# Optimization experiments

Measured on AMD Instinct MI355X. Metric: run time of the kernel, lower is better.

## Reference

```python
import jax, jax.numpy as jnp
import numpy as np
import math

B, S, HID = 2, 2048, 1024
NH = 16
HD = HID // NH  # 64
CHUNK = 128  # min(128, S) from the module


def setup_inputs() -> dict:
    key = jax.random.key(0)
    ks = jax.random.split(key, 8)
    scale = 1.0 / math.sqrt(HID)
    return {
        "hidden_states": jax.random.normal(ks[0], (B, S, HID), jnp.float32),
        "attention_mask": jnp.zeros((B, S, S), jnp.float32),
        "Wq": jax.random.normal(ks[1], (HID, HID), jnp.float32) * scale,
        "bq": jnp.zeros((HID,), jnp.float32),
        "Wk": jax.random.normal(ks[2], (HID, HID), jnp.float32) * scale,
        "bk": jnp.zeros((HID,), jnp.float32),
        "Wv": jax.random.normal(ks[3], (HID, HID), jnp.float32) * scale,
        "bv": jnp.zeros((HID,), jnp.float32),
        "head_weights": jnp.ones((NH,), jnp.float32),
    }


def _split_heads(x):
    # [B,S,HID] -> [B,NH,S,HD]
    b, s, _ = x.shape
    return x.reshape(b, s, NH, HD).transpose(0, 2, 1, 3)


def reference(hidden_states, attention_mask, Wq, bq, Wk, bk, Wv, bv, head_weights):
    # nn.Linear: y = x @ W.T + b
    q = _split_heads(hidden_states @ Wq.T + bq)  # [B,NH,S,HD]
    k = _split_heads(hidden_states @ Wk.T + bk)
    v = _split_heads(hidden_states @ Wv.T + bv)

    scores = jnp.einsum("bhqd,bhkd->bhqk", q, k) / math.sqrt(HD)
    scores = scores + attention_mask[:, None, :, :]  # additive mask broadcast over heads
    probs = jax.nn.softmax(scores, axis=-1)
    # dropout p=0.0 -> identity; post-softmax head-weight scaling (head_pruning)
    probs = probs * head_weights[None, :, None, None]
    ctx = jnp.einsum("bhqk,bhkd->bhqd", probs, v)  # [B,NH,S,HD]
    context_layer = ctx.transpose(0, 2, 1, 3).reshape(B, S, HID)

    # module returns the probs of the LAST query chunk of the python loop
    last_start = ((S + CHUNK - 1) // CHUNK - 1) * CHUNK
    output_attention_probs = probs[:, :, last_start:S, :]  # [B,NH,128,S]
    return context_layer, output_attention_probs
```

## Files before the change

### kernel.cpp

```cpp
#include <hip/hip_runtime.h>

typedef unsigned short u16;
typedef __attribute__((ext_vector_type(8))) short bf16x8;
typedef __attribute__((ext_vector_type(4))) float f32x4;

#define B_   2
#define S_   2048
#define HID_ 1024
#define NH_  16
#define HD_  64
#define SCALE_ 0.125f

__device__ __forceinline__ u16 f2bf(float f) {
    union { float f; unsigned int i; } v; v.f = f;
    unsigned int r = v.i + 0x7fffu + ((v.i >> 16) & 1u);
    return (u16)(r >> 16);
}
__device__ __forceinline__ bf16x8 ld8(const u16* p) {
    return *reinterpret_cast<const bf16x8*>(p);
}
__device__ __forceinline__ unsigned cvtpk(float lo, float hi) {
    unsigned r;
    asm("v_cvt_pk_bf16_f32 %0, %1, %2" : "=v"(r) : "v"(lo), "v"(hi));
    return r;
}
__device__ __forceinline__ void gll16(const u16* g, const u16* l) {
    __builtin_amdgcn_global_load_lds(
        (const __attribute__((address_space(1))) unsigned int*)g,
        (__attribute__((address_space(3))) unsigned int*)l, 16, 0, 0);
}

__global__ __launch_bounds__(256) void conv_scan(
    const float* __restrict__ X, const float* __restrict__ W0,
    const float* __restrict__ W1, const float* __restrict__ W2,
    const unsigned* __restrict__ m,
    u16* __restrict__ Xb, u16* __restrict__ Wb, unsigned* __restrict__ flag)
{
    const int bx = blockIdx.x;
    if (bx < 3584) {
        const size_t s = (size_t)bx * 256 + threadIdx.x;
        const float* src; u16* dst; size_t off;
        if (s < 524288) { src = X; dst = Xb; off = s * 8; }
        else {
            const size_t t = s - 524288;
            const int w = (int)(t >> 17);
            off = (t & 131071) * 8;
            src = w == 0 ? W0 : w == 1 ? W1 : W2;
            dst = Wb + (size_t)w * 1048576;
        }
        f32x4 a = *(const f32x4*)(src + off);
        f32x4 b = *(const f32x4*)(src + off + 4);
        bf16x8 r;
        #pragma unroll
        for (int e = 0; e < 4; e++) { r[e] = (short)f2bf(a[e]); r[4 + e] = (short)f2bf(b[e]); }
        *(bf16x8*)(dst + off) = r;
    } else {
        const size_t i = ((size_t)(bx - 3584) * 256 + threadIdx.x) * 8;
        const uint4* p = (const uint4*)(m + i);
        uint4 a = p[0], b = p[1];
        const unsigned M = 0x7fffffffu;
        unsigned v = (a.x & M) | (a.y & M) | (a.z & M) | (a.w & M)
                   | (b.x & M) | (b.y & M) | (b.z & M) | (b.w & M);
        if (v) atomicOr(flag, 1u);
    }
}

#define BK_ 64

__global__ __launch_bounds__(256) void qkv_mfma(
    const u16* __restrict__ Xb, const u16* __restrict__ Wb,
    const float* __restrict__ bq, const float* __restrict__ bk,
    const float* __restrict__ bv,
    u16* __restrict__ Q, u16* __restrict__ K, u16* __restrict__ V)
{
    __shared__ __align__(16) u16 As[128 * BK_];
    __shared__ __align__(16) u16 Bs[128 * BK_];

    const int tid  = threadIdx.x;
    const int wave = tid >> 6;
    const int lane = tid & 63;
    const int l16  = lane & 15;
    const int quad = lane >> 4;
    const int wr   = wave >> 1, wc = wave & 1;

    const int i0 = blockIdx.x * 128;
    const int j0 = blockIdx.y * 128;

    const int grow = lane >> 3;
    const int gcol = (lane & 7) * 8;

    f32x4 acc[4][4] = {};

    for (int k0 = 0; k0 < HID_; k0 += BK_) {
        __syncthreads();
        #pragma unroll
        for (int g = 0; g < 4; g++) {
            const int u = wave * 4 + g;
            gll16(Xb + (size_t)(i0 + u * 8 + grow) * HID_ + k0 + gcol, As + u * 512);
            gll16(Wb + (size_t)(j0 + u * 8 + grow) * HID_ + k0 + gcol, Bs + u * 512);
        }
        __syncthreads();

        #pragma unroll
        for (int kk = 0; kk < 2; kk++) {
            bf16x8 af[4], bfr[4];
            #pragma unroll
            for (int mt = 0; mt < 4; mt++)
                af[mt] = ld8(&As[(wr * 64 + mt * 16 + l16) * BK_ + kk * 32 + quad * 8]);
            #pragma unroll
            for (int nt = 0; nt < 4; nt++)
                bfr[nt] = ld8(&Bs[(wc * 64 + nt * 16 + l16) * BK_ + kk * 32 + quad * 8]);
            #pragma unroll
            for (int mt = 0; mt < 4; mt++)
                #pragma unroll
                for (int nt = 0; nt < 4; nt++)
                    acc[mt][nt] = __builtin_amdgcn_mfma_f32_16x16x32_bf16(af[mt], bfr[nt], acc[mt][nt], 0, 0, 0);
        }
    }

    const int which = j0 >> 10;
    const float* bias = which == 0 ? bq : which == 1 ? bk : bv;
    u16* Y            = which == 0 ? Q  : which == 1 ? K  : V;

    u16* bb = As + wave * 2048;

    #pragma unroll
    for (int p = 0; p < 2; p++) {
        __syncthreads();
        #pragma unroll
        for (int t2 = 0; t2 < 2; t2++) {
            const int nt = 2 * p + t2;
            const int j  = j0 + wc * 64 + nt * 16 + l16;
            const int jj = j & 1023;
            const float bv_ = bias[jj];
            #pragma unroll
            for (int mt = 0; mt < 4; mt++)
                #pragma unroll
                for (int r = 0; r < 4; r++) {
                    const int row = mt * 16 + quad * 4 + r;
                    const int col = t2 * 16 + l16;
                    const u16 val = f2bf(acc[mt][nt][r] + bv_);
                    if (which == 2)
                        bb[col * 64 + (row ^ ((col & 7) << 3))] = val;
                    else
                        bb[row * 32 + (col ^ ((row & 0xC) << 1))] = val;
                }
        }
        __syncthreads();
        #pragma unroll
        for (int k = 0; k < 4; k++) {
            const int c = lane + 64 * k;
            if (which == 2) {
                const int col  = c >> 3;
                const int row0 = (c & 7) * 8;
                bf16x8 v = ld8(&bb[col * 64 + (row0 ^ ((col & 7) << 3))]);
                const int j  = j0 + wc * 64 + p * 32 + col;
                const int jj = j & 1023;
                const int h = jj >> 6, d = jj & 63;
                const int i = i0 + wr * 64 + row0;
                const int b = i >> 11, s = i & (S_ - 1);
                *(bf16x8*)&Y[((size_t)(b * NH_ + h) * HD_ + d) * S_ + s] = v;
            } else {
                const int row  = c >> 2;
                const int col0 = (c & 3) * 8;
                bf16x8 v = ld8(&bb[row * 32 + (col0 ^ ((row & 0xC) << 1))]);
                const int j  = j0 + wc * 64 + p * 32 + col0;
                const int jj = j & 1023;
                const int h = jj >> 6, d = jj & 63;
                const int i = i0 + wr * 64 + row;
                const int b = i >> 11, s = i & (S_ - 1);
                *(bf16x8*)&Y[(((size_t)(b * NH_ + h) * S_ + s) * HD_) + d] = v;
            }
        }
    }
}

__global__ __launch_bounds__(256) void attn(
    const u16* __restrict__ Q, const u16* __restrict__ K, const u16* __restrict__ Vt,
    const float* __restrict__ mask, const float* __restrict__ hw,
    const unsigned* __restrict__ mflag,
    float* __restrict__ ctx, float* __restrict__ ml)
{
    __shared__ __align__(16) u16 Ks[2][64 * 64];
    __shared__ __align__(16) u16 Vs[2][64 * 64];
    __shared__ __align__(16) u16 Pl[4][16 * 64];

    const int usemask = (mflag[0] != 0);

    const int tid  = threadIdx.x;
    const int wave = tid >> 6;
    const int lane = tid & 63;
    const int l16  = lane & 15;
    const int quad = lane >> 4;
    const int x7   = l16 & 7;

    const int lin = blockIdx.x + 32 * (blockIdx.y + 16 * blockIdx.z);
    const int xcd = lin & 7, jj = lin >> 3;
    const int qb  = jj & 31;
    const int hb  = xcd * 4 + (jj >> 5);
    const int h   = hb & 15, b = hb >> 4;
    const int bh  = b * NH_ + h;

    const u16* Qh  = Q  + (size_t)bh * S_ * HD_;
    const u16* Kh  = K  + (size_t)bh * S_ * HD_;
    const u16* Vth = Vt + (size_t)bh * HD_ * S_;
    const float* Mb = mask + (size_t)b * S_ * S_;

    const int q0 = qb * 64 + wave * 16;

    bf16x8 qf0 = ld8(Qh + (size_t)(q0 + l16) * HD_ + quad * 8);
    bf16x8 qf1 = ld8(Qh + (size_t)(q0 + l16) * HD_ + 32 + quad * 8);

    f32x4 oacc[4] = {};
    float l_part = 0.f;

    const int srow = tid >> 3;
    const int sch  = tid & 7;
    const int ssw  = (sch ^ (srow & 7)) * 8;
    const int sL   = srow * 64 + ssw;

    {
        bf16x8 k0 = ld8(Kh + (size_t)srow * HD_ + sch * 8);
        bf16x8 k1 = ld8(Kh + (size_t)(srow + 32) * HD_ + sch * 8);
        bf16x8 v0 = ld8(Vth + (size_t)srow * S_ + sch * 8);
        bf16x8 v1 = ld8(Vth + (size_t)(srow + 32) * S_ + sch * 8);
        *(bf16x8*)&Ks[0][sL] = k0; *(bf16x8*)&Ks[0][sL + 2048] = k1;
        *(bf16x8*)&Vs[0][sL] = v0; *(bf16x8*)&Vs[0][sL + 2048] = v1;
    }
    __syncthreads();

    for (int t = 0; t < 32; ++t) {
        const int cur = t & 1;
        const int kt  = t * 64;
        const u16* Kb = Ks[cur];
        const u16* Vb = Vs[cur];

        bf16x8 kr0, kr1, vr0, vr1;
        if (t < 31) {
            const u16* Kg = Kh + (size_t)(kt + 64) * HD_;
            kr0 = ld8(Kg + (size_t)srow * HD_ + sch * 8);
            kr1 = ld8(Kg + (size_t)(srow + 32) * HD_ + sch * 8);
            vr0 = ld8(Vth + (size_t)srow * S_ + kt + 64 + sch * 8);
            vr1 = ld8(Vth + (size_t)(srow + 32) * S_ + kt + 64 + sch * 8);
        }

        f32x4 sacc[4] = {};
        __builtin_amdgcn_s_setprio(1);
        #pragma unroll
        for (int nb = 0; nb < 4; nb++) {
            const int base = (nb * 16 + l16) * 64;
            bf16x8 k0 = ld8(&Kb[base + ((quad ^ x7) * 8)]);
            bf16x8 k1 = ld8(&Kb[base + (((quad + 4) ^ x7) * 8)]);
            sacc[nb] = __builtin_amdgcn_mfma_f32_16x16x32_bf16(k0, qf0, sacc[nb], 0, 0, 0);
            sacc[nb] = __builtin_amdgcn_mfma_f32_16x16x32_bf16(k1, qf1, sacc[nb], 0, 0, 0);
        }
        __builtin_amdgcn_s_setprio(0);

        float p[4][4];
        if (usemask) {
            const float* Mrow = Mb + (size_t)(q0 + l16) * S_ + kt;
            #pragma unroll
            for (int nb = 0; nb < 4; nb++) {
                const float4 mv = *(const float4*)(Mrow + nb * 16 + quad * 4);
                p[nb][0] = __expf(fminf(sacc[nb][0] * SCALE_ + mv.x, 80.f));
                p[nb][1] = __expf(fminf(sacc[nb][1] * SCALE_ + mv.y, 80.f));
                p[nb][2] = __expf(fminf(sacc[nb][2] * SCALE_ + mv.z, 80.f));
                p[nb][3] = __expf(fminf(sacc[nb][3] * SCALE_ + mv.w, 80.f));
                l_part += p[nb][0] + p[nb][1] + p[nb][2] + p[nb][3];
            }
        } else {
            #pragma unroll
            for (int nb = 0; nb < 4; nb++) {
                #pragma unroll
                for (int r = 0; r < 4; r++) {
                    p[nb][r] = __expf(fminf(sacc[nb][r] * SCALE_, 80.f));
                    l_part += p[nb][r];
                }
            }
        }

        {
            u16* prow = &Pl[wave][l16 * 64];
            #pragma unroll
            for (int nb = 0; nb < 4; nb++) {
                uint2 w;
                w.x = cvtpk(p[nb][0], p[nb][1]);
                w.y = cvtpk(p[nb][2], p[nb][3]);
                const int ch  = 2 * nb + (quad >> 1);
                const int off = ((ch ^ x7) << 3) + ((quad & 1) << 2);
                *(uint2*)&prow[off] = w;
            }
        }

        __builtin_amdgcn_s_setprio(1);
        #pragma unroll
        for (int kb = 0; kb < 2; kb++) {
            const int c = kb * 4 + quad;
            bf16x8 pf = ld8(&Pl[wave][l16 * 64 + ((c ^ x7) * 8)]);
            #pragma unroll
            for (int db = 0; db < 4; db++) {
                bf16x8 vf = ld8(&Vb[(db * 16 + l16) * 64 + ((c ^ x7) * 8)]);
                oacc[db] = __builtin_amdgcn_mfma_f32_16x16x32_bf16(pf, vf, oacc[db], 0, 0, 0);
            }
        }
        __builtin_amdgcn_s_setprio(0);

        if (t < 31) {
            u16* Kd = Ks[cur ^ 1]; u16* Vd = Vs[cur ^ 1];
            *(bf16x8*)&Kd[sL] = kr0; *(bf16x8*)&Kd[sL + 2048] = kr1;
            *(bf16x8*)&Vd[sL] = vr0; *(bf16x8*)&Vd[sL + 2048] = vr1;
        }
        __syncthreads();
    }

    float lsum = l_part;
    lsum += __shfl_xor(lsum, 16);
    lsum += __shfl_xor(lsum, 32);

    const float hwf  = hw[h];
    const float invq = hwf / lsum;
    float invl[4];
    #pragma unroll
    for (int r = 0; r < 4; r++)
        invl[r] = __shfl(invq, (lane & 48) + quad * 4 + r);

    #pragma unroll
    for (int db = 0; db < 4; db++)
        #pragma unroll
        for (int r = 0; r < 4; r++) {
            const int qrow = q0 + quad * 4 + r;
            ctx[((size_t)(b * S_ + qrow)) * HID_ + h * HD_ + db * 16 + l16] =
                oacc[db][r] * invl[r];
        }

    if (qb >= 30 && quad == 0)
        ml[bh * 128 + (q0 - 1920) + l16] = lsum;
}

__global__ __launch_bounds__(256) void probs_qk(
    const u16* __restrict__ Q, const u16* __restrict__ K,
    const float* __restrict__ mask, const float* __restrict__ hw,
    const unsigned* __restrict__ mflag, const float* __restrict__ ml,
    float* __restrict__ probs_out)
{
    const int usemask = (mflag[0] != 0);

    const int tid  = threadIdx.x;
    const int wave = tid >> 6;
    const int lane = tid & 63;
    const int l16  = lane & 15;
    const int quad = lane >> 4;

    const int rt = blockIdx.x & 1;
    const int ks = blockIdx.x >> 1;
    const int h  = blockIdx.y;
    const int b  = blockIdx.z;
    const int bh = b * NH_ + h;

    const u16* Qh = Q + (size_t)bh * S_ * HD_;
    const u16* Kh = K + (size_t)bh * S_ * HD_;
    const float* Mb = mask + (size_t)b * S_ * S_;

    const int q0   = 1920 + rt * 64 + wave * 16;
    const int qrow = q0 + l16;

    bf16x8 qf0 = ld8(Qh + (size_t)qrow * HD_ + quad * 8);
    bf16x8 qf1 = ld8(Qh + (size_t)qrow * HD_ + 32 + quad * 8);

    const float invl = hw[h] / ml[bh * 128 + (qrow - 1920)];
    float* Prow = probs_out + ((size_t)bh * 128 + (qrow - 1920)) * S_;
    const float* Mrow = Mb + (size_t)qrow * S_;

    for (int kt = ks * 256; kt < ks * 256 + 256; kt += 64) {
        f32x4 sacc[4] = {};
        #pragma unroll
        for (int nb = 0; nb < 4; nb++) {
            const u16* krow = Kh + (size_t)(kt + nb * 16 + l16) * HD_ + quad * 8;
            bf16x8 kA0 = ld8(krow);
            bf16x8 kA1 = ld8(krow + 32);
            sacc[nb] = __builtin_amdgcn_mfma_f32_16x16x32_bf16(kA0, qf0, sacc[nb], 0, 0, 0);
            sacc[nb] = __builtin_amdgcn_mfma_f32_16x16x32_bf16(kA1, qf1, sacc[nb], 0, 0, 0);
        }
        #pragma unroll
        for (int nb = 0; nb < 4; nb++) {
            const int kb0 = kt + nb * 16 + quad * 4;
            float4 v;
            if (usemask) {
                const float4 mv = *(const float4*)&Mrow[kb0];
                v.x = __expf(fminf(sacc[nb][0] * SCALE_ + mv.x, 80.f)) * invl;
                v.y = __expf(fminf(sacc[nb][1] * SCALE_ + mv.y, 80.f)) * invl;
                v.z = __expf(fminf(sacc[nb][2] * SCALE_ + mv.z, 80.f)) * invl;
                v.w = __expf(fminf(sacc[nb][3] * SCALE_ + mv.w, 80.f)) * invl;
            } else {
                v.x = __expf(fminf(sacc[nb][0] * SCALE_, 80.f)) * invl;
                v.y = __expf(fminf(sacc[nb][1] * SCALE_, 80.f)) * invl;
                v.z = __expf(fminf(sacc[nb][2] * SCALE_, 80.f)) * invl;
                v.w = __expf(fminf(sacc[nb][3] * SCALE_, 80.f)) * invl;
            }
            *(float4*)&Prow[kb0] = v;
        }
    }
}

extern "C" void kernel_launch(void* const* d_in, const int* in_sizes, int n_in,
                              void* d_out, int out_size, void* d_ws, size_t ws_size,
                              hipStream_t stream)
{
    const void* X = 0; const void* mask = 0; const void* hw = 0;
    const void* Wm[3] = {0, 0, 0}; const void* bm[3] = {0, 0, 0};
    int wi = 0, bi = 0;
    for (int i = 0; i < n_in; i++) {
        switch (in_sizes[i]) {
            case 4194304: X = d_in[i]; break;
            case 8388608: mask = d_in[i]; break;
            case 1048576: if (wi < 3) Wm[wi++] = d_in[i]; break;
            case 1024:    if (bi < 3) bm[bi++] = d_in[i]; break;
            case 16:      hw = d_in[i]; break;
            default: break;
        }
    }
    if (!X || !mask || wi != 3 || bi != 3 || !hw) {
        X = d_in[0]; mask = d_in[1];
        Wm[0] = d_in[2]; bm[0] = d_in[3];
        Wm[1] = d_in[4]; bm[1] = d_in[5];
        Wm[2] = d_in[6]; bm[2] = d_in[7];
        hw = d_in[8];
    }

    u16* Q  = (u16*)d_ws;
    u16* Kw = Q + 4194304ull;
    u16* Vw = Kw + 4194304ull;
    u16* Xb = Vw + 4194304ull;
    u16* Wb = Xb + 4194304ull;
    unsigned* flag = (unsigned*)(Wb + 3145728ull);
    float* ml = (float*)(flag + 64);

    float* ctx   = (float*)d_out;
    float* probs = ctx + (size_t)B_ * S_ * HID_;

    hipMemsetAsync(flag, 0, 4, stream);
    conv_scan<<<7680, 256, 0, stream>>>(
        (const float*)X, (const float*)Wm[0], (const float*)Wm[1], (const float*)Wm[2],
        (const unsigned*)mask, Xb, Wb, flag);

    qkv_mfma<<<dim3(32, 24), dim3(256), 0, stream>>>(
        Xb, Wb, (const float*)bm[0], (const float*)bm[1], (const float*)bm[2],
        Q, Kw, Vw);

    attn<<<dim3(32, 16, 2), dim3(256), 0, stream>>>(
        Q, Kw, Vw, (const float*)mask, (const float*)hw, flag, ctx, ml);

    probs_qk<<<dim3(16, 16, 2), dim3(256), 0, stream>>>(
        Q, Kw, (const float*)mask, (const float*)hw, flag, ml, probs);
}
```

Before: 241.2 us.

## Swizzle QKV GEMM LDS tiles, fold softmax scale into exp2, split sum accumulators

Applies an XOR swizzle to the global-to-LDS loads and the fragment reads of the QKV projection GEMM to avoid LDS bank conflicts. Softmax exponentials switch from __expf with a separate scale to exp2f with the scale and log2e folded into one constant, saving a multiply per element. The row-sum accumulator becomes four independent partial sums to shorten the dependency chain. The P-tile store is split into two 32-bit writes. The swizzle must match the direct-to-LDS load layout exactly, and the exp2 form changes rounding slightly.

Result: no change. 243.0 us (+0.8%).

```diff
diff --git a/kernel.cpp b/kernel.cpp
--- a/kernel.cpp
+++ b/kernel.cpp
@@ -10,6 +10,9 @@
 #define NH_  16
 #define HD_  64
 #define SCALE_ 0.125f
+#define C2_   0.1803368801111f
+#define CLAMP2_ 115.4156035f
+#define LOG2E_ 1.4426950408890f
 
 __device__ __forceinline__ u16 f2bf(float f) {
     union { float f; unsigned int i; } v; v.f = f;
@@ -81,13 +84,14 @@
     const int lane = tid & 63;
     const int l16  = lane & 15;
     const int quad = lane >> 4;
+    const int x7   = l16 & 7;
     const int wr   = wave >> 1, wc = wave & 1;
 
     const int i0 = blockIdx.x * 128;
     const int j0 = blockIdx.y * 128;
 
     const int grow = lane >> 3;
-    const int gcol = (lane & 7) * 8;
+    const int gsw  = ((lane & 7) ^ grow) * 8;
 
     f32x4 acc[4][4] = {};
 
@@ -96,8 +100,8 @@
         #pragma unroll
         for (int g = 0; g < 4; g++) {
             const int u = wave * 4 + g;
-            gll16(Xb + (size_t)(i0 + u * 8 + grow) * HID_ + k0 + gcol, As + u * 512);
-            gll16(Wb + (size_t)(j0 + u * 8 + grow) * HID_ + k0 + gcol, Bs + u * 512);
+            gll16(Xb + (size_t)(i0 + u * 8 + grow) * HID_ + k0 + gsw, As + u * 512);
+            gll16(Wb + (size_t)(j0 + u * 8 + grow) * HID_ + k0 + gsw, Bs + u * 512);
         }
         __syncthreads();
 
@@ -106,10 +110,10 @@
             bf16x8 af[4], bfr[4];
             #pragma unroll
             for (int mt = 0; mt < 4; mt++)
-                af[mt] = ld8(&As[(wr * 64 + mt * 16 + l16) * BK_ + kk * 32 + quad * 8]);
+                af[mt] = ld8(&As[(wr * 64 + mt * 16 + l16) * BK_ + (((kk * 4 + quad) ^ x7) * 8)]);
             #pragma unroll
             for (int nt = 0; nt < 4; nt++)
-                bfr[nt] = ld8(&Bs[(wc * 64 + nt * 16 + l16) * BK_ + kk * 32 + quad * 8]);
+                bfr[nt] = ld8(&Bs[(wc * 64 + nt * 16 + l16) * BK_ + (((kk * 4 + quad) ^ x7) * 8)]);
             #pragma unroll
             for (int mt = 0; mt < 4; mt++)
                 #pragma unroll
@@ -212,7 +216,7 @@
     bf16x8 qf1 = ld8(Qh + (size_t)(q0 + l16) * HD_ + 32 + quad * 8);
 
     f32x4 oacc[4] = {};
-    float l_part = 0.f;
+    f32x4 lp = {0.f, 0.f, 0.f, 0.f};
 
     const int srow = tid >> 3;
     const int sch  = tid & 7;
@@ -262,19 +266,20 @@
             #pragma unroll
             for (int nb = 0; nb < 4; nb++) {
                 const float4 mv = *(const float4*)(Mrow + nb * 16 + quad * 4);
-                p[nb][0] = __expf(fminf(sacc[nb][0] * SCALE_ + mv.x, 80.f));
-                p[nb][1] = __expf(fminf(sacc[nb][1] * SCALE_ + mv.y, 80.f));
-                p[nb][2] = __expf(fminf(sacc[nb][2] * SCALE_ + mv.z, 80.f));
-                p[nb][3] = __expf(fminf(sacc[nb][3] * SCALE_ + mv.w, 80.f));
-                l_part += p[nb][0] + p[nb][1] + p[nb][2] + p[nb][3];
+                p[nb][0] = exp2f(fminf(fmaf(mv.x, LOG2E_, sacc[nb][0] * C2_), CLAMP2_));
+                p[nb][1] = exp2f(fminf(fmaf(mv.y, LOG2E_, sacc[nb][1] * C2_), CLAMP2_));
+                p[nb][2] = exp2f(fminf(fmaf(mv.z, LOG2E_, sacc[nb][2] * C2_), CLAMP2_));
+                p[nb][3] = exp2f(fminf(fmaf(mv.w, LOG2E_, sacc[nb][3] * C2_), CLAMP2_));
+                #pragma unroll
+                for (int r = 0; r < 4; r++) lp[r] += p[nb][r];
             }
         } else {
             #pragma unroll
             for (int nb = 0; nb < 4; nb++) {
                 #pragma unroll
                 for (int r = 0; r < 4; r++) {
-                    p[nb][r] = __expf(fminf(sacc[nb][r] * SCALE_, 80.f));
-                    l_part += p[nb][r];
+                    p[nb][r] = exp2f(fminf(sacc[nb][r] * C2_, CLAMP2_));
+                    lp[r] += p[nb][r];
                 }
             }
         }
@@ -283,12 +288,12 @@
             u16* prow = &Pl[wave][l16 * 64];
             #pragma unroll
             for (int nb = 0; nb < 4; nb++) {
-                uint2 w;
-                w.x = cvtpk(p[nb][0], p[nb][1]);
-                w.y = cvtpk(p[nb][2], p[nb][3]);
+                const unsigned wx = cvtpk(p[nb][0], p[nb][1]);
+                const unsigned wy = cvtpk(p[nb][2], p[nb][3]);
                 const int ch  = 2 * nb + (quad >> 1);
                 const int off = ((ch ^ x7) << 3) + ((quad & 1) << 2);
-                *(uint2*)&prow[off] = w;
+                *(unsigned*)&prow[off]     = wx;
+                *(unsigned*)&prow[off + 2] = wy;
             }
         }
 
@@ -313,7 +318,7 @@
         __syncthreads();
     }
 
-    float lsum = l_part;
+    float lsum = (lp[0] + lp[1]) + (lp[2] + lp[3]);
     lsum += __shfl_xor(lsum, 16);
     lsum += __shfl_xor(lsum, 32);
 
@@ -387,15 +392,15 @@
             float4 v;
             if (usemask) {
                 const float4 mv = *(const float4*)&Mrow[kb0];
-                v.x = __expf(fminf(sacc[nb][0] * SCALE_ + mv.x, 80.f)) * invl;
-                v.y = __expf(fminf(sacc[nb][1] * SCALE_ + mv.y, 80.f)) * invl;
-                v.z = __expf(fminf(sacc[nb][2] * SCALE_ + mv.z, 80.f)) * invl;
-                v.w = __expf(fminf(sacc[nb][3] * SCALE_ + mv.w, 80.f)) * invl;
+                v.x = exp2f(fminf(fmaf(mv.x, LOG2E_, sacc[nb][0] * C2_), CLAMP2_)) * invl;
+                v.y = exp2f(fminf(fmaf(mv.y, LOG2E_, sacc[nb][1] * C2_), CLAMP2_)) * invl;
+                v.z = exp2f(fminf(fmaf(mv.z, LOG2E_, sacc[nb][2] * C2_), CLAMP2_)) * invl;
+                v.w = exp2f(fminf(fmaf(mv.w, LOG2E_, sacc[nb][3] * C2_), CLAMP2_)) * invl;
             } else {
-                v.x = __expf(fminf(sacc[nb][0] * SCALE_, 80.f)) * invl;
-                v.y = __expf(fminf(sacc[nb][1] * SCALE_, 80.f)) * invl;
-                v.z = __expf(fminf(sacc[nb][2] * SCALE_, 80.f)) * invl;
-                v.w = __expf(fminf(sacc[nb][3] * SCALE_, 80.f)) * invl;
+                v.x = exp2f(fminf(sacc[nb][0] * C2_, CLAMP2_)) * invl;
+                v.y = exp2f(fminf(sacc[nb][1] * C2_, CLAMP2_)) * invl;
+                v.z = exp2f(fminf(sacc[nb][2] * C2_, CLAMP2_)) * invl;
+                v.w = exp2f(fminf(sacc[nb][3] * C2_, CLAMP2_)) * invl;
             }
             *(float4*)&Prow[kb0] = v;
         }
```
